# Kernel tuning notes

Measured on AMD Instinct MI355X. Metric: run time of the kernel, lower is better.

Reference implementation:

```python
import jax, jax.numpy as jnp
import numpy as np

N, F, K_KEEP = 4096, 256, 2048

def setup_inputs() -> dict:
    key = jax.random.key(0)
    k1, k2, k3, k4 = jax.random.split(key, 4)
    X = jax.random.normal(k1, (N, F), dtype=jnp.float32)
    A = jax.random.uniform(k2, (N, N), dtype=jnp.float32)
    S = jnp.sort(jax.random.randint(k3, (N,), 0, 16).astype(jnp.int64))
    kernel = jax.random.normal(k4, (F, 1), dtype=jnp.float32) * (1.0 / np.sqrt(F))
    return {"X": X, "A": A, "S": S, "kernel": kernel}

def reference(X, A, S, kernel):
    # score projection with L2-normalized kernel (normalized over all elements)
    kn = kernel / jnp.sqrt(jnp.sum(kernel * kernel))
    y = X @ kn                                   # (N, 1)
    # top-k node selection; boolean_mask via scatter preserves index order,
    # so gather with sorted indices is exactly equivalent
    _, idx = jax.lax.top_k(y[:, 0], K_KEEP)
    idx = jnp.sort(idx)                          # (k,)
    features = X * jnp.tanh(y)                   # (N, F)
    X_pooled = features[idx]                     # (k, F)
    A2 = A @ A                                   # (N, N) -- preserves connectivity
    A_pooled = A2[idx][:, idx]                   # (k, k)
    S_pooled = S[idx]                            # (k,)
    return X_pooled, A_pooled, S_pooled
```

## Files before the change

### kernel.cpp

```cpp
#include <hip/hip_runtime.h>
#include <hip/hip_bf16.h>


#define NN 4096
#define FF 256
#define KKEEP 2048
#define KDIM 4096

#define BM 256
#define BN 128
#define BK 64
#define LDSBUF 49152

typedef __attribute__((ext_vector_type(8))) short short8;
typedef __attribute__((ext_vector_type(4))) float f32x4;

__device__ __forceinline__ unsigned short f2bf(float x) {
  unsigned u = __float_as_uint(x);
  unsigned r = (u + 0x7FFFu + ((u >> 16) & 1u)) >> 16;
  return (unsigned short)r;
}

__device__ __forceinline__ void gload_lds16(const void* g, void* l) {
  __builtin_amdgcn_global_load_lds((const __attribute__((address_space(1))) void*)g,
                                   (__attribute__((address_space(3))) void*)l, 16, 0, 0);
}

__global__ __launch_bounds__(256) void k_score(const float* __restrict__ X,
                                               const float* __restrict__ kern,
                                               float* __restrict__ y) {
  int t = threadIdx.x, lane = t & 63, w = t >> 6;
  int row = blockIdx.x * 4 + w;
  const float4* X4 = (const float4*)(X + (size_t)row * FF);
  const float4* K4 = (const float4*)kern;
  float4 xv = X4[lane];
  float4 kv = K4[lane];
  float p  = xv.x * kv.x + xv.y * kv.y + xv.z * kv.z + xv.w * kv.w;
  float pk = kv.x * kv.x + kv.y * kv.y + kv.z * kv.z + kv.w * kv.w;
  #pragma unroll
  for (int off = 32; off; off >>= 1) {
    p  += __shfl_xor(p, off);
    pk += __shfl_xor(pk, off);
  }
  if (lane == 0) y[row] = p / sqrtf(pk);
}

__global__ __launch_bounds__(256) void k_rank(const float* __restrict__ y,
                                              int* __restrict__ sel) {
  __shared__ __align__(16) float ys[NN];
  __shared__ int part[4][16];
  int t = threadIdx.x;
  const float4* Y4 = (const float4*)y;
  float4* ys4 = (float4*)ys;
  #pragma unroll
  for (int k = 0; k < 4; ++k) ys4[t + k * 256] = Y4[t + k * 256];
  __syncthreads();
  int lane = t & 63, w = t >> 6;
  int r = lane & 15;
  int i = blockIdx.x * 16 + r;
  int seg = w * 4 + (lane >> 4);
  float yi = ys[i];
  int cnt = 0;
  #pragma unroll 4
  for (int s = 0; s < 64; ++s) {
    int f4 = seg * 64 + ((s + seg * 4) & 63);
    float4 v = ys4[f4];
    int j = f4 * 4;
    cnt += (int)((v.x > yi) || (v.x == yi && (j + 0) < i));
    cnt += (int)((v.y > yi) || (v.y == yi && (j + 1) < i));
    cnt += (int)((v.z > yi) || (v.z == yi && (j + 2) < i));
    cnt += (int)((v.w > yi) || (v.w == yi && (j + 3) < i));
  }
  cnt += __shfl_xor(cnt, 16);
  cnt += __shfl_xor(cnt, 32);
  if (lane < 16) part[w][lane] = cnt;
  __syncthreads();
  if (w == 0 && lane < 16) {
    int tot = part[0][lane] + part[1][lane] + part[2][lane] + part[3][lane];
    sel[blockIdx.x * 16 + lane] = (tot < KKEEP) ? 1 : 0;
  }
}

__global__ __launch_bounds__(256) void k_compact(const int* __restrict__ sel,
                                                 const int* __restrict__ S32,
                                                 int* __restrict__ idxb,
                                                 float* __restrict__ outSf,
                                                 long long* __restrict__ outSi,
                                                 int smode) {
  __shared__ int sums[256];
  __shared__ int offs[256];
  int t = threadIdx.x;
  int base = t * 16;
  int loc[16];
  int s = 0;
  #pragma unroll
  for (int u = 0; u < 16; ++u) { loc[u] = sel[base + u]; s += loc[u]; }
  sums[t] = s;
  __syncthreads();
  if (t == 0) {
    int acc = 0;
    for (int q = 0; q < 256; ++q) { offs[q] = acc; acc += sums[q]; }
  }
  __syncthreads();
  bool in64 = (S32[NN - 1] == 0);
  int pos = offs[t];
  for (int u = 0; u < 16; ++u) {
    if (loc[u]) {
      int gi = base + u;
      idxb[pos] = gi;
      int sval = in64 ? S32[2 * gi] : S32[gi];
      if (smode == 0) outSf[pos] = (float)sval;
      else            outSi[pos] = (long long)sval;
      ++pos;
    }
  }
}

__global__ __launch_bounds__(256) void k_gatherAX(const float* __restrict__ A,
                                                  const float* __restrict__ X,
                                                  const float* __restrict__ y,
                                                  const int* __restrict__ idxb,
                                                  unsigned short* __restrict__ Ag,
                                                  float* __restrict__ outX) {
  int tid = blockIdx.x * 256 + threadIdx.x;
  #pragma unroll
  for (int it = 0; it < 8; ++it) {
    int e = tid + it * 262144;
    int p = e >> 10, c4 = e & 1023;
    int r = idxb[p];
    float4 v = ((const float4*)(A + (size_t)r * NN))[c4];
    ushort4 o;
    o.x = f2bf(v.x); o.y = f2bf(v.y); o.z = f2bf(v.z); o.w = f2bf(v.w);
    ((ushort4*)Ag)[e] = o;
  }
  if (tid < 131072) {
    int p = tid >> 6, c4 = tid & 63;
    int r = idxb[p];
    float ty = tanhf(y[r]);
    float4 v = ((const float4*)(X + (size_t)r * FF))[c4];
    v.x *= ty; v.y *= ty; v.z *= ty; v.w *= ty;
    ((float4*)outX)[tid] = v;
  }
}

__global__ __launch_bounds__(256) void k_packB(const float* __restrict__ A,
                                               const int* __restrict__ idxb,
                                               unsigned short* __restrict__ Bt) {
  __shared__ unsigned short tile[64][66];
  __shared__ int sidx[64];
  int t = threadIdx.x;
  int bk = blockIdx.x & 63;
  int bq = blockIdx.x >> 6;
  int k0 = bk * 64, q0 = bq * 64;
  if (t < 64) sidx[t] = idxb[q0 + t];
  __syncthreads();
  int j = t & 63, i0 = t >> 6;
  #pragma unroll
  for (int rr = 0; rr < 16; ++rr) {
    int i = i0 + rr * 4;
    float v = A[(size_t)(k0 + i) * NN + sidx[j]];
    tile[i][j] = f2bf(v);
  }
  __syncthreads();
  int i2 = t & 63, j0 = t >> 6;
  #pragma unroll
  for (int rr = 0; rr < 16; ++rr) {
    int jj = j0 + rr * 4;
    Bt[(size_t)(q0 + jj) * KDIM + k0 + i2] = tile[i2][jj];
  }
}

__device__ __forceinline__ void stage_rows(const unsigned short* __restrict__ srcbase,
                                           int rowoff, int koff,
                                           char* ldsregion, int j, int t, int w) {
  int p = j * 8192 + t * 16;
  int row = p >> 7;
  int l = p ^ ((row & 7) << 4);
  const unsigned short* src = srcbase + (size_t)(rowoff + row) * KDIM + koff + ((l & 127) >> 1);
  gload_lds16(src, ldsregion + j * 8192 + w * 1024);
}

__global__ __launch_bounds__(512, 2) void k_gemm2(const unsigned short* __restrict__ Ag,
                                                  const unsigned short* __restrict__ Bt,
                                                  float* __restrict__ Cdst, int nt) {
  __shared__ __align__(16) unsigned short lds[3 * LDSBUF / 2];
  int t = threadIdx.x, lane = t & 63, w = t >> 6;
  int bx = blockIdx.x, by = blockIdx.y, z = blockIdx.z;
  int wm = w >> 1, wn = w & 1;
  int fr = lane & 15, fq = lane >> 4;
  int kbase = z * nt * BK;

  f32x4 acc[4][4];
  #pragma unroll
  for (int mf = 0; mf < 4; ++mf)
    #pragma unroll
    for (int nf = 0; nf < 4; ++nf) acc[mf][nf] = f32x4{0.f, 0.f, 0.f, 0.f};

  #pragma unroll
  for (int pt = 0; pt < 2; ++pt) {
    char* bufA = (char*)lds + pt * LDSBUF;
    char* bufB = bufA + 32768;
    int koff = kbase + pt * BK;
    stage_rows(Ag, by * BM, koff, bufA, 0, t, w);
    stage_rows(Ag, by * BM, koff, bufA, 1, t, w);
    stage_rows(Ag, by * BM, koff, bufA, 2, t, w);
    stage_rows(Ag, by * BM, koff, bufA, 3, t, w);
    stage_rows(Bt, bx * BN, koff, bufB, 0, t, w);
    stage_rows(Bt, bx * BN, koff, bufB, 1, t, w);
  }

  int cb = 0;
  for (int kt = 0; kt < nt; ++kt) {
    if (kt == nt - 1) asm volatile("s_waitcnt vmcnt(0)" ::: "memory");
    else              asm volatile("s_waitcnt vmcnt(6)" ::: "memory");
    __builtin_amdgcn_s_barrier();

    int sb = cb + 2; if (sb >= 3) sb -= 3;
    const char* lA = (const char*)lds + cb * LDSBUF;
    const char* lB = lA + 32768;
    char* sA = (char*)lds + sb * LDSBUF;
    char* sB = sA + 32768;
    bool doStage = (kt + 2) < nt;
    int koff2 = kbase + (kt + 2) * BK;

    #pragma unroll
    for (int ksub = 0; ksub < 2; ++ksub) {
      if (doStage) {
        if (ksub == 0) {
          stage_rows(Ag, by * BM, koff2, sA, 0, t, w);
          stage_rows(Ag, by * BM, koff2, sA, 1, t, w);
          stage_rows(Ag, by * BM, koff2, sA, 2, t, w);
        } else {
          stage_rows(Ag, by * BM, koff2, sA, 3, t, w);
          stage_rows(Bt, bx * BN, koff2, sB, 0, t, w);
          stage_rows(Bt, bx * BN, koff2, sB, 1, t, w);
        }
      }
      short8 a[4], b[4];
      #pragma unroll
      for (int mf = 0; mf < 4; ++mf) {
        int r = wm * 64 + mf * 16 + fr;
        int lb = r * 128 + ksub * 64 + fq * 16;
        int pb = lb ^ ((r & 7) << 4);
        a[mf] = *(const short8*)(lA + pb);
      }
      #pragma unroll
      for (int nf = 0; nf < 4; ++nf) {
        int r = wn * 64 + nf * 16 + fr;
        int lb = r * 128 + ksub * 64 + fq * 16;
        int pb = lb ^ ((r & 7) << 4);
        b[nf] = *(const short8*)(lB + pb);
      }
      __builtin_amdgcn_s_setprio(1);
      #pragma unroll
      for (int mf = 0; mf < 4; ++mf)
        #pragma unroll
        for (int nf = 0; nf < 4; ++nf)
          acc[mf][nf] = __builtin_amdgcn_mfma_f32_16x16x32_bf16(a[mf], b[nf], acc[mf][nf], 0, 0, 0);
      __builtin_amdgcn_s_setprio(0);
    }
    __builtin_amdgcn_s_barrier();
    cb = (cb + 1 == 3) ? 0 : cb + 1;
  }

  float* Cp = Cdst + (size_t)z * KKEEP * KKEEP;
  #pragma unroll
  for (int mf = 0; mf < 4; ++mf)
    #pragma unroll
    for (int nf = 0; nf < 4; ++nf)
      #pragma unroll
      for (int rr = 0; rr < 4; ++rr) {
        int row = by * BM + wm * 64 + mf * 16 + fq * 4 + rr;
        int col = bx * BN + wn * 64 + nf * 16 + fr;
        Cp[(size_t)row * KKEEP + col] = acc[mf][nf][rr];
      }
}

__global__ __launch_bounds__(256) void k_reduce(const float* __restrict__ Cpart,
                                                float* __restrict__ outA, int nsplit) {
  const size_t Q = (size_t)KKEEP * KKEEP / 4;
  size_t e = (size_t)blockIdx.x * 256 + threadIdx.x;
  const float4* P = (const float4*)Cpart;
  float4 o = P[e];
  for (int s = 1; s < nsplit; ++s) {
    float4 v = P[e + (size_t)s * Q];
    o.x += v.x; o.y += v.y; o.z += v.z; o.w += v.w;
  }
  ((float4*)outA)[e] = o;
}

extern "C" void kernel_launch(void* const* d_in, const int* in_sizes, int n_in,
                              void* d_out, int out_size, void* d_ws, size_t ws_size,
                              hipStream_t stream) {
  const float* X    = (const float*)d_in[0];
  const float* A    = (const float*)d_in[1];
  const int*   S32  = (const int*)d_in[2];
  const float* kern = (const float*)d_in[3];

  float* out  = (float*)d_out;
  float* outX = out;
  float* outA = out + 2048 * 256;
  float*      outSf = out + 2048 * 256 + 2048 * 2048;
  long long*  outSi = (long long*)((char*)d_out + (size_t)(2048 * 256 + 2048 * 2048) * 4);
  int smode = (out_size == 4722688) ? 1 : 0;

  char* wsb = (char*)d_ws;
  float* y    = (float*)wsb;
  int*   sel  = (int*)(wsb + 16384);
  int*   idxb = (int*)(wsb + 32768);
  unsigned short* Ag = (unsigned short*)(wsb + 65536);
  unsigned short* Bt = Ag + (size_t)KKEEP * KDIM;
  float* Cpart = (float*)(Bt + (size_t)KKEEP * KDIM);

  const size_t PART = (size_t)KKEEP * KKEEP * 4;
  const size_t BASE = 65536 + (size_t)KKEEP * KDIM * 2 * 2;
  int ksplit = (ws_size >= BASE + 2 * PART) ? 2 : 1;
  float* gemmDst = (ksplit > 1) ? Cpart : outA;
  int nt = KDIM / (BK * ksplit);

  hipLaunchKernelGGL(k_score,    dim3(1024),  dim3(256), 0, stream, X, kern, y);
  hipLaunchKernelGGL(k_rank,     dim3(256),   dim3(256), 0, stream, y, sel);
  hipLaunchKernelGGL(k_compact,  dim3(1),     dim3(256), 0, stream, sel, S32, idxb, outSf, outSi, smode);
  hipLaunchKernelGGL(k_gatherAX, dim3(1024),  dim3(256), 0, stream, A, X, y, idxb, Ag, outX);
  hipLaunchKernelGGL(k_packB,    dim3(2048),  dim3(256), 0, stream, A, idxb, Bt);
  hipLaunchKernelGGL(k_gemm2,    dim3(16, 8, ksplit), dim3(512), 0, stream,
                     Ag, Bt, gemmDst, nt);
  if (ksplit > 1)
    hipLaunchKernelGGL(k_reduce, dim3(4096),  dim3(256), 0, stream, Cpart, outA, ksplit);
}
```

Before: 186.2 us.

## Fuse split-K reduction into GEMM epilogue via atomic tickets and remap blocks per XCD

Removes the separate split-K reduce kernel. Each GEMM block writes its partial tile, takes an atomic ticket per output tile, and the second finisher adds the other partial into the final output. It also remaps block IDs so tiles sharing A/B rows land on the same XCD, improving L2 reuse. The cost is an extra fence and atomic per block, plus counters that are zeroed inside the score kernel.

```diff
diff --git a/kernel.cpp b/kernel.cpp
--- a/kernel.cpp
+++ b/kernel.cpp
@@ -28,8 +28,10 @@
 
 __global__ __launch_bounds__(256) void k_score(const float* __restrict__ X,
                                                const float* __restrict__ kern,
-                                               float* __restrict__ y) {
+                                               float* __restrict__ y,
+                                               int* __restrict__ cnt) {
   int t = threadIdx.x, lane = t & 63, w = t >> 6;
+  if (blockIdx.x == 0 && t < 128) cnt[t] = 0;
   int row = blockIdx.x * 4 + w;
   const float4* X4 = (const float4*)(X + (size_t)row * FF);
   const float4* K4 = (const float4*)kern;
@@ -182,10 +184,21 @@
 
 __global__ __launch_bounds__(512, 2) void k_gemm2(const unsigned short* __restrict__ Ag,
                                                   const unsigned short* __restrict__ Bt,
-                                                  float* __restrict__ Cdst, int nt) {
+                                                  float* __restrict__ Cpart,
+                                                  float* __restrict__ outA,
+                                                  int* __restrict__ cnt, int nt) {
   __shared__ __align__(16) unsigned short lds[3 * LDSBUF / 2];
+  __shared__ int ticket;
   int t = threadIdx.x, lane = t & 63, w = t >> 6;
   int bx = blockIdx.x, by = blockIdx.y, z = blockIdx.z;
+  if (gridDim.z == 2) {
+    int bid = bx + by * 16 + z * 128;
+    int xcd = bid & 7, j = bid >> 3;
+    int rem = j & 15;
+    bx = (xcd & 3) * 4 + (rem & 3);
+    by = (xcd >> 2) * 4 + (rem >> 2);
+    z  = j >> 4;
+  }
   int wm = w >> 1, wn = w & 1;
   int fr = lane & 15, fq = lane >> 4;
   int kbase = z * nt * BK;
@@ -263,7 +276,21 @@
     cb = (cb + 1 == 3) ? 0 : cb + 1;
   }
 
-  float* Cp = Cdst + (size_t)z * KKEEP * KKEEP;
+  if (gridDim.z == 1) {
+    #pragma unroll
+    for (int mf = 0; mf < 4; ++mf)
+      #pragma unroll
+      for (int nf = 0; nf < 4; ++nf)
+        #pragma unroll
+        for (int rr = 0; rr < 4; ++rr) {
+          int row = by * BM + wm * 64 + mf * 16 + fq * 4 + rr;
+          int col = bx * BN + wn * 64 + nf * 16 + fr;
+          outA[(size_t)row * KKEEP + col] = acc[mf][nf][rr];
+        }
+    return;
+  }
+
+  float* Cp = Cpart + (size_t)z * KKEEP * KKEEP;
   #pragma unroll
   for (int mf = 0; mf < 4; ++mf)
     #pragma unroll
@@ -274,19 +301,24 @@
         int col = bx * BN + wn * 64 + nf * 16 + fr;
         Cp[(size_t)row * KKEEP + col] = acc[mf][nf][rr];
       }
-}
-
-__global__ __launch_bounds__(256) void k_reduce(const float* __restrict__ Cpart,
-                                                float* __restrict__ outA, int nsplit) {
-  const size_t Q = (size_t)KKEEP * KKEEP / 4;
-  size_t e = (size_t)blockIdx.x * 256 + threadIdx.x;
-  const float4* P = (const float4*)Cpart;
-  float4 o = P[e];
-  for (int s = 1; s < nsplit; ++s) {
-    float4 v = P[e + (size_t)s * Q];
-    o.x += v.x; o.y += v.y; o.z += v.z; o.w += v.w;
-  }
-  ((float4*)outA)[e] = o;
+  __threadfence();
+  __syncthreads();
+  if (t == 0) ticket = atomicAdd(&cnt[by * 16 + bx], 1);
+  __syncthreads();
+  if (ticket == 1) {
+    __threadfence();
+    const float* Co = Cpart + (size_t)(z ^ 1) * KKEEP * KKEEP;
+    #pragma unroll
+    for (int mf = 0; mf < 4; ++mf)
+      #pragma unroll
+      for (int nf = 0; nf < 4; ++nf)
+        #pragma unroll
+        for (int rr = 0; rr < 4; ++rr) {
+          int row = by * BM + wm * 64 + mf * 16 + fq * 4 + rr;
+          int col = bx * BN + wn * 64 + nf * 16 + fr;
+          outA[(size_t)row * KKEEP + col] = acc[mf][nf][rr] + Co[(size_t)row * KKEEP + col];
+        }
+  }
 }
 
 extern "C" void kernel_launch(void* const* d_in, const int* in_sizes, int n_in,
@@ -308,6 +340,7 @@
   float* y    = (float*)wsb;
   int*   sel  = (int*)(wsb + 16384);
   int*   idxb = (int*)(wsb + 32768);
+  int*   cnt  = (int*)(wsb + 40960);
   unsigned short* Ag = (unsigned short*)(wsb + 65536);
   unsigned short* Bt = Ag + (size_t)KKEEP * KDIM;
   float* Cpart = (float*)(Bt + (size_t)KKEEP * KDIM);
@@ -315,16 +348,13 @@
   const size_t PART = (size_t)KKEEP * KKEEP * 4;
   const size_t BASE = 65536 + (size_t)KKEEP * KDIM * 2 * 2;
   int ksplit = (ws_size >= BASE + 2 * PART) ? 2 : 1;
-  float* gemmDst = (ksplit > 1) ? Cpart : outA;
   int nt = KDIM / (BK * ksplit);
 
-  hipLaunchKernelGGL(k_score,    dim3(1024),  dim3(256), 0, stream, X, kern, y);
+  hipLaunchKernelGGL(k_score,    dim3(1024),  dim3(256), 0, stream, X, kern, y, cnt);
   hipLaunchKernelGGL(k_rank,     dim3(256),   dim3(256), 0, stream, y, sel);
   hipLaunchKernelGGL(k_compact,  dim3(1),     dim3(256), 0, stream, sel, S32, idxb, outSf, outSi, smode);
   hipLaunchKernelGGL(k_gatherAX, dim3(1024),  dim3(256), 0, stream, A, X, y, idxb, Ag, outX);
   hipLaunchKernelGGL(k_packB,    dim3(2048),  dim3(256), 0, stream, A, idxb, Bt);
   hipLaunchKernelGGL(k_gemm2,    dim3(16, 8, ksplit), dim3(512), 0, stream,
-                     Ag, Bt, gemmDst, nt);
-  if (ksplit > 1)
-    hipLaunchKernelGGL(k_reduce, dim3(4096),  dim3(256), 0, stream, Cpart, outA, ksplit);
-}
+                     Ag, Bt, Cpart, outA, cnt, nt);
+}
```

Measured after the change: 291.9 us. 56.8% more time.
